# Kernel tuning notes

Measured on AMD Instinct MI355X. Metric: run time of the kernel, lower is better.

## Reference

```python
import jax, jax.numpy as jnp
import numpy as np

NUM_CLASSES = 100
NUM_HYPER_PER = 16
TOPK_RATIO = 0.1
ZDIM = 256
B = 64
K = 128


def setup_inputs() -> dict:
    key = jax.random.key(0)
    k1, k2, k3 = jax.random.split(key, 3)
    x = jax.random.normal(k1, (B, K, ZDIM), dtype=jnp.float32)
    y = jax.random.randint(k2, (B,), 0, NUM_CLASSES)
    hyper_params = jax.random.normal(k3, (NUM_CLASSES, NUM_HYPER_PER, ZDIM), dtype=jnp.float32)
    return {"x": x, "y": y, "hyper_params": hyper_params}


def _generate_G_from_H(H):
    # H: [N_nodes, N_edges], edge weights W = 1
    # G = DV^{-1/2} H DE^{-1} H^T DV^{-1/2}
    DV = H.sum(axis=1)          # node degrees [N]
    DE = H.sum(axis=0)          # edge degrees [E]
    inv_DE = 1.0 / DE
    DV2 = DV ** -0.5
    left = (DV2[:, None] * H) * inv_DE[None, :]   # DV^{-1/2} H DE^{-1}  [N, E]
    right = H * DV2[:, None]                      # (DV^{-1/2} H)       [N, E]
    return left @ right.T                         # [N, N]


def reference(x, y, hyper_params):
    B_, K_, d = x.shape
    # gather per-sample class hyperedge prototypes -> [B*P, d]
    hyper_clss = hyper_params[y].reshape(-1, d)
    # similarity, rearranged '(B K) E' then transposed -> [E, N]
    simi = jnp.einsum('bkd,ed->bke', x, hyper_clss).reshape(B_ * K_, -1).T
    kk = int(TOPK_RATIO * simi.shape[-1])
    # k-th largest similarity per edge as threshold
    thr = jax.lax.top_k(simi, kk)[0][:, -1:]      # [E, 1]
    H = (simi > thr).astype(jnp.float32).T        # incidence [N, E]
    G = _generate_G_from_H(H)
    hyper_x = x.reshape(-1, d)                    # [N, d]
    return (G, hyper_x)
```

## Files before the change

### kernel.cpp

```cpp
#include <hip/hip_runtime.h>
#include <hip/hip_bf16.h>
#include <cstdint>

#define NN 8192
#define EE 1024
#define DD 256
#define KK_SEL 819

typedef __attribute__((ext_vector_type(4))) int int32x4;

__global__ __launch_bounds__(256) void simi_gemm(
    const float* __restrict__ x, const int* __restrict__ y,
    const float* __restrict__ hyper, float* __restrict__ simi) {
  __shared__ float As[16][128];
  __shared__ float Bs[16][128];
  const int tid = threadIdx.x;
  const int bi = blockIdx.y;
  const int bj = blockIdx.x;
  const int ty = tid >> 4, tx = tid & 15;
  float acc[2][4][2][4] = {};

  const int lr = tid >> 1;
  const int lk = (tid & 1) * 8;
  const int eg = bi * 128 + lr;
  const int cls = y[eg >> 4];
  const float* arow = hyper + ((size_t)(cls * 16 + (eg & 15))) * DD;
  const float* brow = x + (size_t)(bj * 128 + lr) * DD;

#pragma unroll 1
  for (int k0 = 0; k0 < DD; k0 += 16) {
    const float4 a0 = *(const float4*)(arow + k0 + lk);
    const float4 a1 = *(const float4*)(arow + k0 + lk + 4);
    const float4 b0 = *(const float4*)(brow + k0 + lk);
    const float4 b1 = *(const float4*)(brow + k0 + lk + 4);
    As[lk + 0][lr] = a0.x; As[lk + 1][lr] = a0.y;
    As[lk + 2][lr] = a0.z; As[lk + 3][lr] = a0.w;
    As[lk + 4][lr] = a1.x; As[lk + 5][lr] = a1.y;
    As[lk + 6][lr] = a1.z; As[lk + 7][lr] = a1.w;
    Bs[lk + 0][lr] = b0.x; Bs[lk + 1][lr] = b0.y;
    Bs[lk + 2][lr] = b0.z; Bs[lk + 3][lr] = b0.w;
    Bs[lk + 4][lr] = b1.x; Bs[lk + 5][lr] = b1.y;
    Bs[lk + 6][lr] = b1.z; Bs[lk + 7][lr] = b1.w;
    __syncthreads();
#pragma unroll
    for (int kk = 0; kk < 16; ++kk) {
      const float4 ar0 = *(const float4*)&As[kk][ty * 4];
      const float4 ar1 = *(const float4*)&As[kk][64 + ty * 4];
      const float4 bc0 = *(const float4*)&Bs[kk][tx * 4];
      const float4 bc1 = *(const float4*)&Bs[kk][64 + tx * 4];
      const float av[2][4] = {{ar0.x, ar0.y, ar0.z, ar0.w},
                              {ar1.x, ar1.y, ar1.z, ar1.w}};
      const float bv[2][4] = {{bc0.x, bc0.y, bc0.z, bc0.w},
                              {bc1.x, bc1.y, bc1.z, bc1.w}};
#pragma unroll
      for (int rh = 0; rh < 2; ++rh)
#pragma unroll
        for (int i = 0; i < 4; ++i)
#pragma unroll
          for (int ch = 0; ch < 2; ++ch)
#pragma unroll
            for (int j = 0; j < 4; ++j)
              acc[rh][i][ch][j] += av[rh][i] * bv[ch][j];
    }
    __syncthreads();
  }
#pragma unroll
  for (int rh = 0; rh < 2; ++rh)
#pragma unroll
    for (int i = 0; i < 4; ++i) {
      const int e = bi * 128 + rh * 64 + ty * 4 + i;
#pragma unroll
      for (int ch = 0; ch < 2; ++ch) {
        float4 o = {acc[rh][i][ch][0], acc[rh][i][ch][1],
                    acc[rh][i][ch][2], acc[rh][i][ch][3]};
        *(float4*)&simi[(size_t)e * NN + bj * 128 + ch * 64 + tx * 4] = o;
      }
    }
}

__global__ __launch_bounds__(256) void select_thr(
    const float* __restrict__ simi, float* __restrict__ thr, int* __restrict__ DE) {
  const int e = blockIdx.x;
  const float* row = simi + (size_t)e * NN;
  __shared__ unsigned hist[256];
  __shared__ unsigned sh_prefix;
  __shared__ int sh_r, sh_less, sh_eq;
  const int tid = threadIdx.x;
  if (tid == 0) { sh_prefix = 0u; sh_r = NN - KK_SEL; sh_less = 0; sh_eq = 0; }
  __syncthreads();

  for (int pass = 0; pass < 4; ++pass) {
    const int shift = 24 - pass * 8;
    hist[tid] = 0u;
    __syncthreads();
    const unsigned prefix = sh_prefix;
    const unsigned pmask = (pass == 0) ? 0u : (0xFFFFFFFFu << (shift + 8));
    for (int i = tid; i < NN; i += 256) {
      unsigned u = __float_as_uint(row[i]);
      unsigned k = (u & 0x80000000u) ? ~u : (u | 0x80000000u);
      if ((k & pmask) == prefix) atomicAdd(&hist[(k >> shift) & 0xFFu], 1u);
    }
    __syncthreads();
    if (tid == 0) {
      unsigned cum = 0;
      int r = sh_r;
      for (int b = 0; b < 256; ++b) {
        unsigned h = hist[b];
        if (cum + h > (unsigned)r) {
          sh_prefix = sh_prefix | ((unsigned)b << shift);
          sh_r = r - (int)cum;
          sh_less += (int)cum;
          if (pass == 3) sh_eq = (int)h;
          break;
        }
        cum += h;
      }
    }
    __syncthreads();
  }
  if (tid == 0) {
    const unsigned key = sh_prefix;
    const unsigned u = (key & 0x80000000u) ? (key & 0x7FFFFFFFu) : ~key;
    thr[e] = __uint_as_float(u);
    DE[e] = NN - sh_less - sh_eq;
  }
}

__global__ __launch_bounds__(256) void build_h(
    const float* __restrict__ simi, const float* __restrict__ thr,
    unsigned long long* __restrict__ Hbits, float* __restrict__ DV2) {
  __shared__ float sthr[EE];
  const int tid = threadIdx.x;
  for (int e = tid; e < EE; e += 256) sthr[e] = thr[e];
  __syncthreads();
  const int n = blockIdx.x * 256 + tid;
  int dv = 0;
#pragma unroll 1
  for (int w = 0; w < 16; ++w) {
    unsigned long long m = 0ull;
#pragma unroll 8
    for (int b = 0; b < 64; ++b) {
      const int e = w * 64 + b;
      const float v = simi[(size_t)e * NN + n];
      m |= ((unsigned long long)(v > sthr[e])) << b;
    }
    Hbits[(size_t)n * 16 + w] = m;
    dv += __popcll(m);
  }
  DV2[n] = 1.0f / sqrtf((float)dv);
}

__global__ __launch_bounds__(256) void h8_expand(
    const unsigned long long* __restrict__ Hbits, unsigned char* __restrict__ H8) {
  const int idx = blockIdx.x * 256 + threadIdx.x;
  const int n = idx >> 6;
  const int c16 = idx & 63;
  const unsigned long long w = Hbits[(size_t)n * 16 + (c16 >> 2)];
  const unsigned int b16 = (unsigned int)((w >> ((c16 & 3) * 16)) & 0xFFFFull);
  uint4 u;
  u.x = ((b16 >> 0) & 1u) | (((b16 >> 1) & 1u) << 8) | (((b16 >> 2) & 1u) << 16) | (((b16 >> 3) & 1u) << 24);
  u.y = ((b16 >> 4) & 1u) | (((b16 >> 5) & 1u) << 8) | (((b16 >> 6) & 1u) << 16) | (((b16 >> 7) & 1u) << 24);
  u.z = ((b16 >> 8) & 1u) | (((b16 >> 9) & 1u) << 8) | (((b16 >> 10) & 1u) << 16) | (((b16 >> 11) & 1u) << 24);
  u.w = ((b16 >> 12) & 1u) | (((b16 >> 13) & 1u) << 8) | (((b16 >> 14) & 1u) << 16) | (((b16 >> 15) & 1u) << 24);
  *(uint4*)(H8 + (size_t)n * EE + c16 * 16) = u;
}

__global__ __launch_bounds__(256) void mode_exc(
    const int* __restrict__ DE, int* __restrict__ modeInfo,
    int* __restrict__ exc_idx, float* __restrict__ exc_delta) {
  __shared__ unsigned hist[1024];
  __shared__ int s_mode;
  __shared__ int s_cnt;
  const int tid = threadIdx.x;
  for (int i = tid; i < 1024; i += 256) hist[i] = 0u;
  __syncthreads();
  for (int e = tid; e < EE; e += 256) atomicAdd(&hist[DE[e]], 1u);
  __syncthreads();
  if (tid == 0) {
    int best = 1; unsigned bc = 0;
    for (int i = 0; i < 1024; ++i)
      if (hist[i] > bc) { bc = hist[i]; best = i; }
    s_mode = best; s_cnt = 0;
  }
  __syncthreads();
  const int mode = s_mode;
  const float invMode = 1.0f / (float)mode;
  for (int e = tid; e < EE; e += 256) {
    const int de = DE[e];
    if (de != mode) {
      const int idx = atomicAdd(&s_cnt, 1);
      exc_idx[idx] = e;
      exc_delta[idx] = 1.0f / (float)de - invMode;
    }
  }
  __syncthreads();
  if (tid == 0) {
    modeInfo[0] = s_mode;
    modeInfo[1] = s_cnt;
    modeInfo[2] = __float_as_int(invMode);
  }
}

__global__ __launch_bounds__(256) void g_mfma(
    const unsigned char* __restrict__ H8, const float* __restrict__ DV2,
    const int* __restrict__ modeInfo, const int* __restrict__ exc_idx,
    const float* __restrict__ exc_delta,
    const unsigned long long* __restrict__ Hbits, float* __restrict__ G) {
  __shared__ unsigned char smem[32768];
  __shared__ float sDVr[128], sDVc[128];
  unsigned char* As = smem;
  unsigned char* Bs = smem + 16384;

  const int t = blockIdx.x;
  int bi = (int)(64.5 - sqrt(64.5 * 64.5 - 2.0 * (double)t));
  while ((bi + 1) * 64 - ((bi + 1) * bi) / 2 <= t) ++bi;
  while (bi * 64 - (bi * (bi - 1)) / 2 > t) --bi;
  const int bj = bi + (t - (bi * 64 - (bi * (bi - 1)) / 2));

  const int tid = threadIdx.x;
  const int lane = tid & 63;
  const int wave = tid >> 6;
  if (tid < 128) sDVr[tid] = DV2[bi * 128 + tid];
  else sDVc[tid - 128] = DV2[bj * 128 + (tid - 128)];

  const unsigned char* Ag = H8 + (size_t)bi * 128 * EE;
  const unsigned char* Bg = H8 + (size_t)bj * 128 * EE;

  int32x4 acc[4][4];
  const int32x4 zero = {0, 0, 0, 0};
#pragma unroll
  for (int m = 0; m < 4; ++m)
#pragma unroll
    for (int n = 0; n < 4; ++n) acc[m][n] = zero;

  const int wr = wave >> 1, wc = wave & 1;

  for (int s = 0; s < 8; ++s) {
    const int kbase = s * 128;
#pragma unroll
    for (int q = 0; q < 4; ++q) {
      const int chunk = wave * 256 + q * 64 + lane;
      const int r = chunk >> 3;
      const int cq = (chunk & 7) * 16;
      const int csrc = cq ^ ((r & 7) << 4);
      __builtin_amdgcn_global_load_lds(
          (const __attribute__((address_space(1))) void*)(Ag + (size_t)r * EE + kbase + csrc),
          (__attribute__((address_space(3))) void*)(As + (wave * 256 + q * 64) * 16),
          16, 0, 0);
      __builtin_amdgcn_global_load_lds(
          (const __attribute__((address_space(1))) void*)(Bg + (size_t)r * EE + kbase + csrc),
          (__attribute__((address_space(3))) void*)(Bs + (wave * 256 + q * 64) * 16),
          16, 0, 0);
    }
    __syncthreads();
#pragma unroll
    for (int ks = 0; ks < 2; ++ks) {
      int32x4 af[4], bf[4];
#pragma unroll
      for (int m = 0; m < 4; ++m) {
        const int r = wr * 64 + m * 16 + (lane & 15);
        const int c = ks * 64 + (lane >> 4) * 16;
        af[m] = *(const int32x4*)&As[r * 128 + (c ^ ((r & 7) << 4))];
      }
#pragma unroll
      for (int n = 0; n < 4; ++n) {
        const int r = wc * 64 + n * 16 + (lane & 15);
        const int c = ks * 64 + (lane >> 4) * 16;
        bf[n] = *(const int32x4*)&Bs[r * 128 + (c ^ ((r & 7) << 4))];
      }
#pragma unroll
      for (int m = 0; m < 4; ++m)
#pragma unroll
        for (int n = 0; n < 4; ++n)
          acc[m][n] = __builtin_amdgcn_mfma_i32_16x16x64_i8(af[m], bf[n], acc[m][n], 0, 0, 0);
    }
    __syncthreads();
  }

  const float invMode = __int_as_float(modeInfo[2]);
  const int NX = modeInfo[1];
  const int l4 = lane >> 4;
  const int lc = lane & 15;

#pragma unroll
  for (int m = 0; m < 4; ++m) {
#pragma unroll
    for (int n = 0; n < 4; ++n) {
#pragma unroll
      for (int reg = 0; reg < 4; ++reg) {
        const int Rl = wr * 64 + m * 16 + l4 * 4 + reg;
        const int Cl = wc * 64 + n * 16 + lc;
        const int Rg = bi * 128 + Rl;
        const int Cg = bj * 128 + Cl;
        float v = (float)acc[m][n][reg] * invMode;
        for (int xx = 0; xx < NX; ++xx) {
          const int e = exc_idx[xx];
          const int w = e >> 6, b = e & 63;
          const unsigned long long rb = Hbits[(size_t)Rg * 16 + w] >> b;
          const unsigned long long cb = Hbits[(size_t)Cg * 16 + w] >> b;
          v += exc_delta[xx] * (float)(rb & cb & 1ull);
        }
        G[(size_t)Rg * NN + Cg] = v * sDVr[Rl] * sDVc[Cl];
      }
    }
  }

  if (bi != bj) {
    float* T = (float*)smem;
#pragma unroll 1
    for (int h = 0; h < 2; ++h) {
      __syncthreads();
      if (wr == h) {
#pragma unroll
        for (int m = 0; m < 4; ++m) {
#pragma unroll
          for (int n = 0; n < 4; ++n) {
#pragma unroll
            for (int reg = 0; reg < 4; ++reg) {
              const int Rh = m * 16 + l4 * 4 + reg;
              const int Cl = wc * 64 + n * 16 + lc;
              float v = (float)acc[m][n][reg] * invMode;
              if (NX) {
                const int Rg = bi * 128 + h * 64 + Rh;
                const int Cg = bj * 128 + Cl;
                for (int xx = 0; xx < NX; ++xx) {
                  const int e = exc_idx[xx];
                  const int w = e >> 6, b = e & 63;
                  const unsigned long long rb = Hbits[(size_t)Rg * 16 + w] >> b;
                  const unsigned long long cb = Hbits[(size_t)Cg * 16 + w] >> b;
                  v += exc_delta[xx] * (float)(rb & cb & 1ull);
                }
              }
              T[Rh * 128 + (Cl ^ ((Rh & 7) << 2))] =
                  v * sDVc[Cl] * sDVr[h * 64 + Rh];
            }
          }
        }
      }
      __syncthreads();
      const int orow = tid >> 1;
      const int ob = (tid & 1) * 32;
      float4* dst = (float4*)&G[(size_t)(bj * 128 + orow) * NN + bi * 128 + h * 64 + ob];
#pragma unroll
      for (int i = 0; i < 8; ++i) {
        const int rr = ob + i * 4;
        float4 o;
        o.x = T[(rr + 0) * 128 + (orow ^ (((rr + 0) & 7) << 2))];
        o.y = T[(rr + 1) * 128 + (orow ^ (((rr + 1) & 7) << 2))];
        o.z = T[(rr + 2) * 128 + (orow ^ (((rr + 2) & 7) << 2))];
        o.w = T[(rr + 3) * 128 + (orow ^ (((rr + 3) & 7) << 2))];
        dst[i] = o;
      }
    }
  }
}

extern "C" void kernel_launch(void* const* d_in, const int* in_sizes, int n_in,
                              void* d_out, int out_size, void* d_ws, size_t ws_size,
                              hipStream_t stream) {
  const float* x = (const float*)d_in[0];
  const int* y = (const int*)d_in[1];
  const float* hyper = (const float*)d_in[2];
  float* out = (float*)d_out;

  float* simi = out;
  unsigned char* H8 = (unsigned char*)(out + (size_t)NN * NN);

  uint8_t* w8 = (uint8_t*)d_ws;
  float* thr = (float*)(w8 + 0);
  int* DE = (int*)(w8 + 4096);
  float* DV2 = (float*)(w8 + 8192);
  int* modeInfo = (int*)(w8 + 40960);
  int* exc_idx = (int*)(w8 + 41984);
  float* exc_delta = (float*)(w8 + 46080);
  unsigned long long* Hbits = (unsigned long long*)(w8 + 65536);

  simi_gemm<<<dim3(NN / 128, EE / 128), 256, 0, stream>>>(x, y, hyper, simi);
  select_thr<<<dim3(EE), 256, 0, stream>>>(simi, thr, DE);
  build_h<<<dim3(NN / 256), 256, 0, stream>>>(simi, thr, Hbits, DV2);
  h8_expand<<<dim3(NN * 64 / 256), 256, 0, stream>>>(Hbits, H8);
  mode_exc<<<dim3(1), 256, 0, stream>>>(DE, modeInfo, exc_idx, exc_delta);
  g_mfma<<<dim3(2080), 256, 0, stream>>>(H8, DV2, modeInfo, exc_idx, exc_delta,
                                         Hbits, out);
  hipMemcpyAsync(out + (size_t)NN * NN, x, (size_t)NN * DD * sizeof(float),
                 hipMemcpyDeviceToDevice, stream);
}
```

Measured before the change: 619.2 us.

## Cache select rows in LDS, parallel prefix scan, fuse H build and byte expansion

select_thr now loads each simi row once into LDS as radix keys, so the four histogram passes no longer re-read global memory. The serial single-thread bucket search is replaced by a block-wide Hillis-Steele prefix scan. build_h and h8_expand are fused into one 2D-grid kernel that writes both Hbits and the byte matrix H8; it emits per-slice partial degrees that g_mfma sums to get DV^-1/2. Costs are 32KB of LDS per select block, which may lower occupancy, plus extra syncs in the scan and partial-degree reads in g_mfma.

Result: faster. 511.9 us (-17.3%).

```diff
diff --git a/kernel.cpp b/kernel.cpp
--- a/kernel.cpp
+++ b/kernel.cpp
@@ -80,12 +80,26 @@
 
 __global__ __launch_bounds__(256) void select_thr(
     const float* __restrict__ simi, float* __restrict__ thr, int* __restrict__ DE) {
-  const int e = blockIdx.x;
-  const float* row = simi + (size_t)e * NN;
+  __shared__ unsigned keys[NN];
   __shared__ unsigned hist[256];
   __shared__ unsigned sh_prefix;
   __shared__ int sh_r, sh_less, sh_eq;
+  const int e = blockIdx.x;
+  const float* row = simi + (size_t)e * NN;
   const int tid = threadIdx.x;
+
+#pragma unroll
+  for (int j = 0; j < 8; ++j) {
+    const int idx = (j * 256 + tid) * 4;
+    const float4 v = *(const float4*)&row[idx];
+    uint4 t;
+    unsigned u;
+    u = __float_as_uint(v.x); t.x = (u & 0x80000000u) ? ~u : (u | 0x80000000u);
+    u = __float_as_uint(v.y); t.y = (u & 0x80000000u) ? ~u : (u | 0x80000000u);
+    u = __float_as_uint(v.z); t.z = (u & 0x80000000u) ? ~u : (u | 0x80000000u);
+    u = __float_as_uint(v.w); t.w = (u & 0x80000000u) ? ~u : (u | 0x80000000u);
+    *(uint4*)&keys[idx] = t;
+  }
   if (tid == 0) { sh_prefix = 0u; sh_r = NN - KK_SEL; sh_less = 0; sh_eq = 0; }
   __syncthreads();
 
@@ -94,27 +108,32 @@
     hist[tid] = 0u;
     __syncthreads();
     const unsigned prefix = sh_prefix;
+    const int r = sh_r;
     const unsigned pmask = (pass == 0) ? 0u : (0xFFFFFFFFu << (shift + 8));
-    for (int i = tid; i < NN; i += 256) {
-      unsigned u = __float_as_uint(row[i]);
-      unsigned k = (u & 0x80000000u) ? ~u : (u | 0x80000000u);
-      if ((k & pmask) == prefix) atomicAdd(&hist[(k >> shift) & 0xFFu], 1u);
-    }
-    __syncthreads();
-    if (tid == 0) {
-      unsigned cum = 0;
-      int r = sh_r;
-      for (int b = 0; b < 256; ++b) {
-        unsigned h = hist[b];
-        if (cum + h > (unsigned)r) {
-          sh_prefix = sh_prefix | ((unsigned)b << shift);
-          sh_r = r - (int)cum;
-          sh_less += (int)cum;
-          if (pass == 3) sh_eq = (int)h;
-          break;
-        }
-        cum += h;
-      }
+#pragma unroll
+    for (int j = 0; j < 8; ++j) {
+      const uint4 kv = *(const uint4*)&keys[(j * 256 + tid) * 4];
+      if ((kv.x & pmask) == prefix) atomicAdd(&hist[(kv.x >> shift) & 0xFFu], 1u);
+      if ((kv.y & pmask) == prefix) atomicAdd(&hist[(kv.y >> shift) & 0xFFu], 1u);
+      if ((kv.z & pmask) == prefix) atomicAdd(&hist[(kv.z >> shift) & 0xFFu], 1u);
+      if ((kv.w & pmask) == prefix) atomicAdd(&hist[(kv.w >> shift) & 0xFFu], 1u);
+    }
+    __syncthreads();
+    const unsigned h = hist[tid];
+#pragma unroll
+    for (int off = 1; off < 256; off <<= 1) {
+      const unsigned add = (tid >= off) ? hist[tid - off] : 0u;
+      __syncthreads();
+      hist[tid] += add;
+      __syncthreads();
+    }
+    const unsigned inc = hist[tid];
+    const unsigned exc = inc - h;
+    if ((int)exc <= r && r < (int)inc) {
+      sh_prefix = prefix | ((unsigned)tid << shift);
+      sh_r = r - (int)exc;
+      sh_less += (int)exc;
+      if (pass == 3) sh_eq = (int)h;
     }
     __syncthreads();
   }
@@ -126,43 +145,43 @@
   }
 }
 
-__global__ __launch_bounds__(256) void build_h(
+__global__ __launch_bounds__(256) void build_h8(
     const float* __restrict__ simi, const float* __restrict__ thr,
-    unsigned long long* __restrict__ Hbits, float* __restrict__ DV2) {
-  __shared__ float sthr[EE];
+    unsigned long long* __restrict__ Hbits, int* __restrict__ DVpart,
+    unsigned char* __restrict__ H8) {
+  __shared__ float sthr[128];
   const int tid = threadIdx.x;
-  for (int e = tid; e < EE; e += 256) sthr[e] = thr[e];
-  __syncthreads();
-  const int n = blockIdx.x * 256 + tid;
+  const int nblk = blockIdx.x;
+  const int by = blockIdx.y;
+  const int e0 = by * 128;
+  if (tid < 128) sthr[tid] = thr[e0 + tid];
+  __syncthreads();
+  const int n = nblk * 256 + tid;
   int dv = 0;
 #pragma unroll 1
-  for (int w = 0; w < 16; ++w) {
+  for (int w2 = 0; w2 < 2; ++w2) {
+    const int w = by * 2 + w2;
     unsigned long long m = 0ull;
 #pragma unroll 8
     for (int b = 0; b < 64; ++b) {
-      const int e = w * 64 + b;
-      const float v = simi[(size_t)e * NN + n];
-      m |= ((unsigned long long)(v > sthr[e])) << b;
+      const int el = w2 * 64 + b;
+      const float v = simi[(size_t)(e0 + el) * NN + n];
+      m |= ((unsigned long long)(v > sthr[el])) << b;
     }
     Hbits[(size_t)n * 16 + w] = m;
     dv += __popcll(m);
-  }
-  DV2[n] = 1.0f / sqrtf((float)dv);
-}
-
-__global__ __launch_bounds__(256) void h8_expand(
-    const unsigned long long* __restrict__ Hbits, unsigned char* __restrict__ H8) {
-  const int idx = blockIdx.x * 256 + threadIdx.x;
-  const int n = idx >> 6;
-  const int c16 = idx & 63;
-  const unsigned long long w = Hbits[(size_t)n * 16 + (c16 >> 2)];
-  const unsigned int b16 = (unsigned int)((w >> ((c16 & 3) * 16)) & 0xFFFFull);
-  uint4 u;
-  u.x = ((b16 >> 0) & 1u) | (((b16 >> 1) & 1u) << 8) | (((b16 >> 2) & 1u) << 16) | (((b16 >> 3) & 1u) << 24);
-  u.y = ((b16 >> 4) & 1u) | (((b16 >> 5) & 1u) << 8) | (((b16 >> 6) & 1u) << 16) | (((b16 >> 7) & 1u) << 24);
-  u.z = ((b16 >> 8) & 1u) | (((b16 >> 9) & 1u) << 8) | (((b16 >> 10) & 1u) << 16) | (((b16 >> 11) & 1u) << 24);
-  u.w = ((b16 >> 12) & 1u) | (((b16 >> 13) & 1u) << 8) | (((b16 >> 14) & 1u) << 16) | (((b16 >> 15) & 1u) << 24);
-  *(uint4*)(H8 + (size_t)n * EE + c16 * 16) = u;
+#pragma unroll
+    for (int jq = 0; jq < 4; ++jq) {
+      const unsigned b16 = (unsigned)((m >> (jq * 16)) & 0xFFFFull);
+      uint4 u;
+      u.x = ((b16 >> 0) & 1u) | (((b16 >> 1) & 1u) << 8) | (((b16 >> 2) & 1u) << 16) | (((b16 >> 3) & 1u) << 24);
+      u.y = ((b16 >> 4) & 1u) | (((b16 >> 5) & 1u) << 8) | (((b16 >> 6) & 1u) << 16) | (((b16 >> 7) & 1u) << 24);
+      u.z = ((b16 >> 8) & 1u) | (((b16 >> 9) & 1u) << 8) | (((b16 >> 10) & 1u) << 16) | (((b16 >> 11) & 1u) << 24);
+      u.w = ((b16 >> 12) & 1u) | (((b16 >> 13) & 1u) << 8) | (((b16 >> 14) & 1u) << 16) | (((b16 >> 15) & 1u) << 24);
+      *(uint4*)(H8 + (size_t)n * EE + w * 64 + jq * 16) = u;
+    }
+  }
+  DVpart[by * NN + n] = dv;
 }
 
 __global__ __launch_bounds__(256) void mode_exc(
@@ -202,7 +221,7 @@
 }
 
 __global__ __launch_bounds__(256) void g_mfma(
-    const unsigned char* __restrict__ H8, const float* __restrict__ DV2,
+    const unsigned char* __restrict__ H8, const int* __restrict__ DVpart,
     const int* __restrict__ modeInfo, const int* __restrict__ exc_idx,
     const float* __restrict__ exc_delta,
     const unsigned long long* __restrict__ Hbits, float* __restrict__ G) {
@@ -220,8 +239,17 @@
   const int tid = threadIdx.x;
   const int lane = tid & 63;
   const int wave = tid >> 6;
-  if (tid < 128) sDVr[tid] = DV2[bi * 128 + tid];
-  else sDVc[tid - 128] = DV2[bj * 128 + (tid - 128)];
+  if (tid < 128) {
+    int dv = 0;
+#pragma unroll
+    for (int s = 0; s < 8; ++s) dv += DVpart[s * NN + bi * 128 + tid];
+    sDVr[tid] = 1.0f / sqrtf((float)dv);
+  } else {
+    int dv = 0;
+#pragma unroll
+    for (int s = 0; s < 8; ++s) dv += DVpart[s * NN + bj * 128 + (tid - 128)];
+    sDVc[tid - 128] = 1.0f / sqrtf((float)dv);
+  }
 
   const unsigned char* Ag = H8 + (size_t)bi * 128 * EE;
   const unsigned char* Bg = H8 + (size_t)bj * 128 * EE;
@@ -369,18 +397,17 @@
   uint8_t* w8 = (uint8_t*)d_ws;
   float* thr = (float*)(w8 + 0);
   int* DE = (int*)(w8 + 4096);
-  float* DV2 = (float*)(w8 + 8192);
-  int* modeInfo = (int*)(w8 + 40960);
-  int* exc_idx = (int*)(w8 + 41984);
-  float* exc_delta = (float*)(w8 + 46080);
-  unsigned long long* Hbits = (unsigned long long*)(w8 + 65536);
+  int* DVpart = (int*)(w8 + 8192);
+  int* modeInfo = (int*)(w8 + 270336);
+  int* exc_idx = (int*)(w8 + 271360);
+  float* exc_delta = (float*)(w8 + 275456);
+  unsigned long long* Hbits = (unsigned long long*)(w8 + 294912);
 
   simi_gemm<<<dim3(NN / 128, EE / 128), 256, 0, stream>>>(x, y, hyper, simi);
   select_thr<<<dim3(EE), 256, 0, stream>>>(simi, thr, DE);
-  build_h<<<dim3(NN / 256), 256, 0, stream>>>(simi, thr, Hbits, DV2);
-  h8_expand<<<dim3(NN * 64 / 256), 256, 0, stream>>>(Hbits, H8);
+  build_h8<<<dim3(32, 8), 256, 0, stream>>>(simi, thr, Hbits, DVpart, H8);
   mode_exc<<<dim3(1), 256, 0, stream>>>(DE, modeInfo, exc_idx, exc_delta);
-  g_mfma<<<dim3(2080), 256, 0, stream>>>(H8, DV2, modeInfo, exc_idx, exc_delta,
+  g_mfma<<<dim3(2080), 256, 0, stream>>>(H8, DVpart, modeInfo, exc_idx, exc_delta,
                                          Hbits, out);
   hipMemcpyAsync(out + (size_t)NN * NN, x, (size_t)NN * DD * sizeof(float),
                  hipMemcpyDeviceToDevice, stream);
```
